# Optimization experiments

Hardware: AMD Instinct MI355X
Metric: run time of the kernel (lower is better)

Reference implementation:

```python
import jax, jax.numpy as jnp
import numpy as np

EPS = 1e-5
K = 1  # kernel_size; forced to 1 by the module's channel bookkeeping (see notes)


def conv2d(x, w, stride=1, padding=0):
    return jax.lax.conv_general_dilated(
        x, w, (stride, stride), [(padding, padding), (padding, padding)],
        dimension_numbers=('NCHW', 'OIHW', 'NCHW'))


def bn_eval(x, g, b):
    # eval-mode BatchNorm2d with running_mean=0, running_var=1
    scale = g * np.float32(1.0 / np.sqrt(1.0 + EPS))
    return x * scale.reshape(1, -1, 1, 1) + b.reshape(1, -1, 1, 1)


def spdconv(x, w, g, b):
    # SPDConv: 2x2 space-to-depth -> conv (bias=False) -> BN -> SiLU
    s2d = jnp.concatenate([x[..., ::2, ::2], x[..., 1::2, ::2],
                           x[..., ::2, 1::2], x[..., 1::2, 1::2]], axis=1)
    return jax.nn.silu(bn_eval(conv2d(s2d, w), g, b))


def fourier_split(x):
    # Fourierforward(J=1): zero-pad to next pow2, rfft2, split low/high bands
    h, w = x.shape[-2], x.shape[-1]
    ph = 1 << int(np.ceil(np.log2(h)))
    pw = 1 << int(np.ceil(np.log2(w)))
    xp = jnp.pad(x, ((0, 0), (0, 0), (0, ph - h), (0, pw - w)))
    f = jnp.fft.rfft2(xp)
    low = f[:, :, :h // 2 + 1, :w // 2 + 1]
    high = f[:, :, h // 2 + 1:h + 1, :w // 2 + 1]
    return low.real, low.imag, high.real, high.imag


def sdi(x, w, b):
    # SDI1: per-sample (unbatched) 3x3 conv, then cumulative product over the batch dim
    y = conv2d(x, w, padding=1) + b.reshape(1, -1, 1, 1)
    return jnp.cumprod(y, axis=0)


def fourier_sdi(x, sdi_w, sdi_b, fuse_w, fuse_g, fuse_b):
    yl, y1, y2, y3 = fourier_split(x)
    parts = [sdi(t, sdi_w, sdi_b) for t in (yl, y1, y2, y3)]
    cat = jnp.concatenate(parts, axis=1)  # (b, 4, h', w')
    return jax.nn.silu(bn_eval(conv2d(cat, fuse_w), fuse_g, fuse_b))


def _forward(x, w_spd_gw, bn_g_gw, bn_b_gw, sdi_w_gw, sdi_b_gw, fuse_w_gw, fuse_g_gw, fuse_b_gw,
             w_spd_gf, bn_g_gf, bn_b_gf, sdi_w_gf, sdi_b_gf, fuse_w_gf, fuse_g_gf, fuse_b_gf,
             gen_g, gen_b, w_final):
    b, c = x.shape[0], x.shape[1]
    # get_weight branch: SPDConv(1x1) -> Fourier_SDIModel
    weight = fourier_sdi(spdconv(x, w_spd_gw, bn_g_gw, bn_b_gw),
                         sdi_w_gw, sdi_b_gw, fuse_w_gw, fuse_g_gw, fuse_b_gw)
    h, w = weight.shape[2], weight.shape[3]
    weighted = jax.nn.softmax(weight.reshape(b, c * c, K * K, h, w), axis=2)
    # generate_feature branch: SPDConv(k) -> Fourier_SDIModel -> BN -> ReLU
    feat = fourier_sdi(spdconv(x, w_spd_gf, bn_g_gf, bn_b_gf),
                       sdi_w_gf, sdi_b_gf, fuse_w_gf, fuse_g_gf, fuse_b_gf)
    feat = jax.nn.relu(bn_eval(feat, gen_g, gen_b)).reshape(b, c * c, K * K, h, w)
    wd = feat * weighted
    # rearrange 'b c (n1 n2) h w -> b c (h n1) (w n2)'
    conv_data = wd.reshape(b, c * c, K, K, h, w).transpose(0, 1, 4, 2, 5, 3)
    conv_data = conv_data.reshape(b, c * c, h * K, w * K)
    # final conv: kernel K, stride autopad(K, p=K)=K (passed as stride arg), no bias
    return conv2d(conv_data, w_final, stride=K)


def setup_inputs() -> dict:
    key = jax.random.key(0)
    ks = jax.random.split(key, 24)
    n = lambda i, shape, s=1.0: jax.random.normal(ks[i], shape, dtype=jnp.float32) * s
    # sdi 3x3 weights scaled ~1/(fft_magnitude*taps) so the cumulative product over
    # the batch dim stays in fp32 range.
    return {
        'x': n(0, (16, 1, 1022, 1022)),
        'w_spd_gw': n(1, (1, 4, 1, 1), 0.5),
        'bn_g_gw': 1.0 + n(2, (1,), 0.1),
        'bn_b_gw': n(3, (1,), 0.1),
        'sdi_w_gw': n(4, (1, 1, 3, 3), 5e-4),
        'sdi_b_gw': n(5, (1,), 0.01),
        'fuse_w_gw': n(6, (1, 4, 1, 1), 0.3),
        'fuse_g_gw': 1.0 + n(7, (1,), 0.1),
        'fuse_b_gw': n(8, (1,), 0.1),
        'w_spd_gf': n(9, (1, 4, 1, 1), 0.5),
        'bn_g_gf': 1.0 + n(10, (1,), 0.1),
        'bn_b_gf': n(11, (1,), 0.1),
        'sdi_w_gf': n(12, (1, 1, 3, 3), 5e-4),
        'sdi_b_gf': n(13, (1,), 0.01),
        'fuse_w_gf': n(14, (1, 4, 1, 1), 0.3),
        'fuse_g_gf': 1.0 + n(15, (1,), 0.1),
        'fuse_b_gf': n(16, (1,), 0.1),
        'gen_g': 1.0 + n(17, (1,), 0.1),
        'gen_b': n(18, (1,), 0.1),
        'w_final': n(19, (64, 1, 1, 1), 0.1),
    }


def reference(x, w_spd_gw, bn_g_gw, bn_b_gw, sdi_w_gw, sdi_b_gw, fuse_w_gw, fuse_g_gw, fuse_b_gw,
              w_spd_gf, bn_g_gf, bn_b_gf, sdi_w_gf, sdi_b_gf, fuse_w_gf, fuse_g_gf, fuse_b_gf,
              gen_g, gen_b, w_final):
    return _forward(x, w_spd_gw, bn_g_gw, bn_b_gw, sdi_w_gw, sdi_b_gw, fuse_w_gw, fuse_g_gw, fuse_b_gw,
                    w_spd_gf, bn_g_gf, bn_b_gf, sdi_w_gf, sdi_b_gf, fuse_w_gf, fuse_g_gf, fuse_b_gf,
                    gen_g, gen_b, w_final)
```

## Files before the change

kernel.cpp:

```cpp
#include <hip/hip_runtime.h>
#include <math.h>


#define PI_F 3.14159265358979323846f

struct cpx { float re, im; };
__device__ __forceinline__ cpx cadd(cpx a, cpx b){ return {a.re+b.re, a.im+b.im}; }
__device__ __forceinline__ cpx csub(cpx a, cpx b){ return {a.re-b.re, a.im-b.im}; }
__device__ __forceinline__ cpx cmul(cpx a, cpx b){ return {a.re*b.re - a.im*b.im, a.re*b.im + a.im*b.re}; }
__device__ __forceinline__ cpx cnegi(cpx a){ return {a.im, -a.re}; }

__device__ __forceinline__ void dft8_dif(cpx* a) {
    const float C = 0.70710678118654752440f;
    cpx t0=cadd(a[0],a[4]), t1=cadd(a[1],a[5]), t2=cadd(a[2],a[6]), t3=cadd(a[3],a[7]);
    cpx s0=csub(a[0],a[4]), s1=csub(a[1],a[5]), s2=csub(a[2],a[6]), s3=csub(a[3],a[7]);
    s1 = (cpx){ C*(s1.re + s1.im), C*(s1.im - s1.re) };
    s2 = cnegi(s2);
    s3 = (cpx){ C*(s3.im - s3.re), -C*(s3.re + s3.im) };
    cpx u0=cadd(t0,t2), u1=cadd(t1,t3), u2=csub(t0,t2), u3=cnegi(csub(t1,t3));
    cpx v0=cadd(s0,s2), v1=cadd(s1,s3), v2=csub(s0,s2), v3=cnegi(csub(s1,s3));
    a[0]=cadd(u0,u1); a[1]=csub(u0,u1); a[2]=cadd(u2,u3); a[3]=csub(u2,u3);
    a[4]=cadd(v0,v1); a[5]=csub(v0,v1); a[6]=cadd(v2,v3); a[7]=csub(v2,v3);
}

__device__ __forceinline__ void twiddle_brev(cpx* a, cpx p) {
    cpx w = p;
    a[4] = cmul(a[4], w); w = cmul(w, p);
    a[2] = cmul(a[2], w); w = cmul(w, p);
    a[6] = cmul(a[6], w); w = cmul(w, p);
    a[1] = cmul(a[1], w); w = cmul(w, p);
    a[5] = cmul(a[5], w); w = cmul(w, p);
    a[3] = cmul(a[3], w); w = cmul(w, p);
    a[7] = cmul(a[7], w);
}

__device__ __forceinline__ void fft512_r8(cpx* a, float* bR, float* bI, int t) {
    float sn, cs;
    dft8_dif(a);
    __sincosf(-2.0f * PI_F * (float)t / 512.0f, &sn, &cs);
    twiddle_brev(a, (cpx){cs, sn});
    bR[0*69 + t] = a[0].re; bI[0*69 + t] = a[0].im;
    bR[4*69 + t] = a[1].re; bI[4*69 + t] = a[1].im;
    bR[2*69 + t] = a[2].re; bI[2*69 + t] = a[2].im;
    bR[6*69 + t] = a[3].re; bI[6*69 + t] = a[3].im;
    bR[1*69 + t] = a[4].re; bI[1*69 + t] = a[4].im;
    bR[5*69 + t] = a[5].re; bI[5*69 + t] = a[5].im;
    bR[3*69 + t] = a[6].re; bI[3*69 + t] = a[6].im;
    bR[7*69 + t] = a[7].re; bI[7*69 + t] = a[7].im;
    __syncthreads();
    int k0 = t & 7, t0 = t >> 3;
    cpx b[8];
#pragma unroll
    for (int i = 0; i < 8; i++) {
        b[i].re = bR[k0*69 + t0 + 8*i];
        b[i].im = bI[k0*69 + t0 + 8*i];
    }
    __syncthreads();
    dft8_dif(b);
    __sincosf(-2.0f * PI_F * (float)t0 / 64.0f, &sn, &cs);
    twiddle_brev(b, (cpx){cs, sn});
    bR[(0*8 + k0)*9 + t0] = b[0].re; bI[(0*8 + k0)*9 + t0] = b[0].im;
    bR[(4*8 + k0)*9 + t0] = b[1].re; bI[(4*8 + k0)*9 + t0] = b[1].im;
    bR[(2*8 + k0)*9 + t0] = b[2].re; bI[(2*8 + k0)*9 + t0] = b[2].im;
    bR[(6*8 + k0)*9 + t0] = b[3].re; bI[(6*8 + k0)*9 + t0] = b[3].im;
    bR[(1*8 + k0)*9 + t0] = b[4].re; bI[(1*8 + k0)*9 + t0] = b[4].im;
    bR[(5*8 + k0)*9 + t0] = b[5].re; bI[(5*8 + k0)*9 + t0] = b[5].im;
    bR[(3*8 + k0)*9 + t0] = b[6].re; bI[(3*8 + k0)*9 + t0] = b[6].im;
    bR[(7*8 + k0)*9 + t0] = b[7].re; bI[(7*8 + k0)*9 + t0] = b[7].im;
    __syncthreads();
    int rowb = t * 9;
#pragma unroll
    for (int i = 0; i < 8; i++) {
        a[i].re = bR[rowb + i];
        a[i].im = bI[rowb + i];
    }
    __syncthreads();
    dft8_dif(a);
}

__global__ __launch_bounds__(512) void fft_rows_spd8(
        const float* __restrict__ x, const float* __restrict__ w4,
        const float* __restrict__ g1, const float* __restrict__ b1,
        float2* __restrict__ RT) {
    __shared__ __align__(16) float pool[9216];
    int tid = threadIdx.x;
    int w = tid >> 6, t = tid & 63;
    float* bR = pool + w * 1152;
    float* bI = bR + 576;
    int row = blockIdx.x * 8 + w;
    int b = row >> 9, yy = row & 511;
    float w0 = w4[0], w1 = w4[1], w2c = w4[2], w3 = w4[3];
    float scale = g1[0] * rsqrtf(1.f + 1e-5f);
    float bias  = b1[0];
    cpx a[8];
#pragma unroll
    for (int m = 0; m < 8; m++) {
        int p = t + 64 * m;
        float v = 0.f;
        if (yy < 511 && p < 511) {
            const float* r0 = x + ((size_t)b * 1022 + 2 * yy) * 1022 + 2 * p;
            float2 e = *(const float2*)r0;
            float2 o = *(const float2*)(r0 + 1022);
            v = w0 * e.x + w1 * o.x + w2c * e.y + w3 * o.y;
            v = v * scale + bias;
            v = v / (1.f + expf(-v));
        }
        a[m] = (cpx){v, 0.f};
    }
    fft512_r8(a, bR, bI, t);
    float2* tile = (float2*)pool;
    tile[(t +   0) * 9 + w] = make_float2(a[0].re, a[0].im);
    tile[(t +  64) * 9 + w] = make_float2(a[4].re, a[4].im);
    tile[(t + 128) * 9 + w] = make_float2(a[2].re, a[2].im);
    tile[(t + 192) * 9 + w] = make_float2(a[6].re, a[6].im);
    __syncthreads();
    int y0 = (blockIdx.x & 63) * 8;
    float2* dst = RT + (size_t)(b * 256) * 512 + y0;
#pragma unroll
    for (int r = 0; r < 4; r++) {
        int e = tid + 512 * r;
        int k = e >> 3, ww = e & 7;
        dst[(size_t)k * 512 + ww] = tile[k * 9 + ww];
    }
}

__global__ __launch_bounds__(512) void fft_cols8(
        const float2* __restrict__ RT, float* __restrict__ tpl) {
    __shared__ __align__(16) float pool[9216];
    int tid = threadIdx.x;
    int w = tid >> 6, t = tid & 63;
    float* bR = pool + w * 1152;
    float* bI = bR + 576;
    int b = blockIdx.x >> 5;
    int kx0 = (blockIdx.x & 31) * 8;
    const float2* src = RT + (size_t)(b * 256 + kx0 + w) * 512;
    cpx a[8];
#pragma unroll
    for (int m = 0; m < 8; m++) {
        float2 v = src[t + 64 * m];
        a[m] = (cpx){v.x, v.y};
    }
    fft512_r8(a, bR, bI, t);
    float2* tile = (float2*)pool;
    tile[(t +   0) * 9 + w] = make_float2(a[0].re, a[0].im);
    tile[(t +  64) * 9 + w] = make_float2(a[4].re, a[4].im);
    tile[(t + 128) * 9 + w] = make_float2(a[2].re, a[2].im);
    tile[(t + 192) * 9 + w] = make_float2(a[6].re, a[6].im);
    tile[(t + 256) * 9 + w] = make_float2(a[1].re, a[1].im);
    tile[(t + 320) * 9 + w] = make_float2(a[5].re, a[5].im);
    tile[(t + 384) * 9 + w] = make_float2(a[3].re, a[3].im);
    tile[(t + 448) * 9 + w] = make_float2(a[7].re, a[7].im);
    __syncthreads();
    const size_t P = (size_t)16 * 256 * 256;
#pragma unroll
    for (int r = 0; r < 8; r++) {
        int e = tid + 512 * r;
        int ky = e >> 3, ww = e & 7;
        float2 v = tile[ky * 9 + ww];
        if (ky < 256) {
            size_t idx = (size_t)(b * 256 + ky) * 256 + kx0 + ww;
            tpl[idx]     = v.x;
            tpl[P + idx] = v.y;
        } else {
            size_t idx = (size_t)(b * 256 + (ky - 256)) * 256 + kx0 + ww;
            tpl[2*P + idx] = v.x;
            tpl[3*P + idx] = v.y;
        }
    }
}

__global__ __launch_bounds__(256) void conv_cum_expand(
        const float* __restrict__ tpl,
        const float* __restrict__ sdiw, const float* __restrict__ sdib,
        const float* __restrict__ fw, const float* __restrict__ fg,
        const float* __restrict__ fb, const float* __restrict__ gg,
        const float* __restrict__ gb, const float* __restrict__ wf,
        float* __restrict__ out) {
    __shared__ float tile[4][18][20];
    int tt  = threadIdx.x;
    int og  = blockIdx.x & 1;
    int tix = blockIdx.x >> 1;
    int ti0 = (tix >> 4) * 16, tj0 = (tix & 15) * 16;
    int tin = tt >> 4, tjn = tt & 15;
    int gi_c = ti0 + tin, gj_c = tj0 + tjn;

    float w9[9];
#pragma unroll
    for (int k = 0; k < 9; k++) w9[k] = sdiw[k];
    float bias = sdib[0];
    float inv = rsqrtf(1.f + 1e-5f);
    float fscale = fg[0] * inv, fbias = fb[0];
    float gscale = gg[0] * inv, gbias = gb[0];
    float fw4[4] = {fw[0], fw[1], fw[2], fw[3]};
    float wfv[32];
#pragma unroll
    for (int oo = 0; oo < 32; oo++) wfv[oo] = wf[og * 32 + oo];

    const size_t P = (size_t)16 * 65536;
    float p[4] = {1.f, 1.f, 1.f, 1.f};
    float* obase = out + (size_t)gi_c * 256 + gj_c;

    for (int b = 0; b < 16; b++) {
#pragma unroll
        for (int it = 0; it < 6; it++) {
            int id = it * 256 + tt;
            if (id < 1296) {
                int c  = id / 324;
                int rm = id - c * 324;
                int r  = rm / 18;
                int cc = rm - r * 18;
                int gi = ti0 + r - 1, gj = tj0 + cc - 1;
                float v = 0.f;
                if (gi >= 0 && gi < 256 && gj >= 0 && gj < 256)
                    v = tpl[c * P + (size_t)b * 65536 + gi * 256 + gj];
                tile[c][r][cc] = v;
            }
        }
        __syncthreads();
        float f = 0.f;
#pragma unroll
        for (int c = 0; c < 4; c++) {
            float acc = bias;
#pragma unroll
            for (int di = 0; di < 3; di++)
#pragma unroll
                for (int dj = 0; dj < 3; dj++)
                    acc += w9[di * 3 + dj] * tile[c][tin + di][tjn + dj];
            p[c] *= acc;
            f += fw4[c] * p[c];
        }
        float bn = f * fscale + fbias;
        float ft = bn / (1.f + expf(-bn));
        float g  = ft * gscale + gbias;
        float f2 = fmaxf(g, 0.f);
        float* ob = obase + (size_t)(b * 64 + og * 32) * 65536;
#pragma unroll
        for (int oo = 0; oo < 32; oo++)
            ob[(size_t)oo * 65536] = f2 * wfv[oo];
        __syncthreads();
    }
}

extern "C" void kernel_launch(void* const* d_in, const int* in_sizes, int n_in,
                              void* d_out, int out_size, void* d_ws, size_t ws_size,
                              hipStream_t stream) {
    const float* x    = (const float*)d_in[0];
    const float* wspd = (const float*)d_in[9];
    const float* bng  = (const float*)d_in[10];
    const float* bnb  = (const float*)d_in[11];
    const float* sdiw = (const float*)d_in[12];
    const float* sdib = (const float*)d_in[13];
    const float* fw   = (const float*)d_in[14];
    const float* fg   = (const float*)d_in[15];
    const float* fb   = (const float*)d_in[16];
    const float* gg   = (const float*)d_in[17];
    const float* gb   = (const float*)d_in[18];
    const float* wf   = (const float*)d_in[19];
    float* out = (float*)d_out;

    float2* RT  = (float2*)d_ws;
    float*  tpl = (float*)d_ws + (size_t)4 * 1024 * 1024;

    fft_rows_spd8  <<<dim3(1024), dim3(512), 0, stream>>>(x, wspd, bng, bnb, RT);
    fft_cols8      <<<dim3(512),  dim3(512), 0, stream>>>(RT, tpl);
    conv_cum_expand<<<dim3(512),  dim3(256), 0, stream>>>(tpl, sdiw, sdib, fw, fg,
                                                          fb, gg, gb, wf, out);
}
```

Measured before the change: 402.1 us.

## Double-buffer SDI tile loads and separate conv phase from output store phase

```diff
diff --git a/kernel.cpp b/kernel.cpp
--- a/kernel.cpp
+++ b/kernel.cpp
@@ -176,68 +176,94 @@
         const float* __restrict__ fb, const float* __restrict__ gg,
         const float* __restrict__ gb, const float* __restrict__ wf,
         float* __restrict__ out) {
-    __shared__ float tile[4][18][20];
+    __shared__ float tile[2][4][18][20];
     int tt  = threadIdx.x;
     int og  = blockIdx.x & 1;
     int tix = blockIdx.x >> 1;
     int ti0 = (tix >> 4) * 16, tj0 = (tix & 15) * 16;
     int tin = tt >> 4, tjn = tt & 15;
-    int gi_c = ti0 + tin, gj_c = tj0 + tjn;
+
+    int goff[6], loff[6];
+#pragma unroll
+    for (int it = 0; it < 6; it++) {
+        int id = it * 256 + tt;
+        int c  = id / 324;
+        int rm = id - c * 324;
+        int r  = rm / 18;
+        int cc = rm - r * 18;
+        int gi = ti0 + r - 1, gj = tj0 + cc - 1;
+        bool in_tile = (id < 1296);
+        bool ok = in_tile && gi >= 0 && gi < 256 && gj >= 0 && gj < 256;
+        goff[it] = ok ? (c * 1048576 + gi * 256 + gj) : -1;
+        loff[it] = in_tile ? ((c * 18 + r) * 20 + cc) : -1;
+    }
 
     float w9[9];
 #pragma unroll
     for (int k = 0; k < 9; k++) w9[k] = sdiw[k];
     float bias = sdib[0];
+    float fw4[4] = {fw[0], fw[1], fw[2], fw[3]};
+
+    float r6[6];
+#pragma unroll
+    for (int it = 0; it < 6; it++)
+        r6[it] = (goff[it] >= 0) ? tpl[goff[it]] : 0.f;
+    {
+        float* dst = &tile[0][0][0][0];
+#pragma unroll
+        for (int it = 0; it < 6; it++)
+            if (loff[it] >= 0) dst[loff[it]] = r6[it];
+    }
+
+    float yreg[16][4];
+    for (int b = 0; b < 16; b++) {
+        if (b < 15) {
+            int boff = (b + 1) * 65536;
+#pragma unroll
+            for (int it = 0; it < 6; it++)
+                r6[it] = (goff[it] >= 0) ? tpl[goff[it] + boff] : 0.f;
+        }
+        __syncthreads();
+        const float (*tb)[18][20] = tile[b & 1];
+#pragma unroll
+        for (int c = 0; c < 4; c++) {
+            float acc = bias;
+#pragma unroll
+            for (int di = 0; di < 3; di++)
+#pragma unroll
+                for (int dj = 0; dj < 3; dj++)
+                    acc += w9[di * 3 + dj] * tb[c][tin + di][tjn + dj];
+            yreg[b][c] = acc;
+        }
+        if (b < 15) {
+            float* dst = &tile[(b + 1) & 1][0][0][0];
+#pragma unroll
+            for (int it = 0; it < 6; it++)
+                if (loff[it] >= 0) dst[loff[it]] = r6[it];
+        }
+    }
+
+    float wreg[32];
+#pragma unroll
+    for (int oo = 0; oo < 32; oo++) wreg[oo] = wf[og * 32 + oo];
     float inv = rsqrtf(1.f + 1e-5f);
     float fscale = fg[0] * inv, fbias = fb[0];
     float gscale = gg[0] * inv, gbias = gb[0];
-    float fw4[4] = {fw[0], fw[1], fw[2], fw[3]};
-    float wfv[32];
-#pragma unroll
-    for (int oo = 0; oo < 32; oo++) wfv[oo] = wf[og * 32 + oo];
-
-    const size_t P = (size_t)16 * 65536;
-    float p[4] = {1.f, 1.f, 1.f, 1.f};
-    float* obase = out + (size_t)gi_c * 256 + gj_c;
-
+    float p0 = 1.f, p1 = 1.f, p2 = 1.f, p3 = 1.f;
+    float* obase = out + (size_t)(og * 32) * 65536
+                 + (size_t)(ti0 + tin) * 256 + (tj0 + tjn);
+#pragma unroll
     for (int b = 0; b < 16; b++) {
-#pragma unroll
-        for (int it = 0; it < 6; it++) {
-            int id = it * 256 + tt;
-            if (id < 1296) {
-                int c  = id / 324;
-                int rm = id - c * 324;
-                int r  = rm / 18;
-                int cc = rm - r * 18;
-                int gi = ti0 + r - 1, gj = tj0 + cc - 1;
-                float v = 0.f;
-                if (gi >= 0 && gi < 256 && gj >= 0 && gj < 256)
-                    v = tpl[c * P + (size_t)b * 65536 + gi * 256 + gj];
-                tile[c][r][cc] = v;
-            }
-        }
-        __syncthreads();
-        float f = 0.f;
-#pragma unroll
-        for (int c = 0; c < 4; c++) {
-            float acc = bias;
-#pragma unroll
-            for (int di = 0; di < 3; di++)
-#pragma unroll
-                for (int dj = 0; dj < 3; dj++)
-                    acc += w9[di * 3 + dj] * tile[c][tin + di][tjn + dj];
-            p[c] *= acc;
-            f += fw4[c] * p[c];
-        }
+        p0 *= yreg[b][0]; p1 *= yreg[b][1]; p2 *= yreg[b][2]; p3 *= yreg[b][3];
+        float f  = fw4[0] * p0 + fw4[1] * p1 + fw4[2] * p2 + fw4[3] * p3;
         float bn = f * fscale + fbias;
         float ft = bn / (1.f + expf(-bn));
         float g  = ft * gscale + gbias;
         float f2 = fmaxf(g, 0.f);
-        float* ob = obase + (size_t)(b * 64 + og * 32) * 65536;
+        float* ob = obase + (size_t)(b * 64) * 65536;
 #pragma unroll
         for (int oo = 0; oo < 32; oo++)
-            ob[(size_t)oo * 65536] = f2 * wfv[oo];
-        __syncthreads();
+            __builtin_nontemporal_store(f2 * wreg[oo], ob + (size_t)oo * 65536);
     }
 }
 
```

Result: no change. 408.7 us (+1.6%).
